# Optimization experiments

Measured on AMD Instinct MI355X. Metric: run time of the kernel, lower is better.

The kernel has to match this reference:

```python
import jax, jax.numpy as jnp
import numpy as np

EPS = 1e-5  # nn.LayerNorm default
H = 16      # n_heads

def _ln(x, s, b):
    m = x.mean(-1, keepdims=True)
    v = x.var(-1, keepdims=True)
    return (x - m) / jnp.sqrt(v + EPS) * s + b


def setup_inputs() -> dict:
    key = jax.random.key(0)
    B, T, D, L, V = 2, 1024, 1024, 6, 32000
    ks = jax.random.split(key, 10)
    def n(k, shape):
        return jax.random.normal(k, shape, dtype=jnp.float32) * 0.02
    return dict(
        x=jax.random.randint(ks[0], (B, T), 0, V),
        tok_emb=n(ks[1], (V, D)),
        pos_emb=n(ks[2], (T, D)),
        Wq=n(ks[3], (L, D, D)), bq=jnp.zeros((L, D), jnp.float32),
        Wk=n(ks[4], (L, D, D)), bk=jnp.zeros((L, D), jnp.float32),
        Wv=n(ks[5], (L, D, D)), bv=jnp.zeros((L, D), jnp.float32),
        ln1_s=jnp.ones((L, D), jnp.float32), ln1_b=jnp.zeros((L, D), jnp.float32),
        W1=n(ks[6], (L, D, 4 * D)), b1=jnp.zeros((L, 4 * D), jnp.float32),
        W2=n(ks[7], (L, 4 * D, D)), b2=jnp.zeros((L, D), jnp.float32),
        ln2_s=jnp.ones((L, D), jnp.float32), ln2_b=jnp.zeros((L, D), jnp.float32),
        Wout=n(ks[8], (D, V)), bout=jnp.zeros((V,), jnp.float32),
    )


def reference(x, tok_emb, pos_emb, Wq, bq, Wk, bk, Wv, bv, ln1_s, ln1_b,
              W1, b1, W2, b2, ln2_s, ln2_b, Wout, bout):
    B, T = x.shape
    D = tok_emb.shape[1]
    hd = D // H
    # embeddings (dropout = identity in eval)
    h = tok_emb[x] + pos_emb[:T]
    # additive causal mask: +1.0 on allowed (tril ones kept), -inf elsewhere,
    # exactly matching torch's tril-ones masked_fill mask
    tril = jnp.tril(jnp.ones((T, T), dtype=h.dtype))
    mask = jnp.where(tril == 0, -jnp.inf, 1.0).astype(h.dtype)
    scale = jnp.asarray(1.0 / np.sqrt(hd), h.dtype)

    def block(h, p):
        wq, bq_, wk, bk_, wv, bv_, l1s, l1b, w1, b1_, w2, b2_, l2s, l2b = p
        def heads(W, b):  # [B,T,D] -> [B,H,T,hd]
            return (h @ W + b).reshape(B, T, H, hd).transpose(0, 2, 1, 3)
        q, k, v = heads(wq, bq_), heads(wk, bk_), heads(wv, bv_)
        s = jnp.einsum('bhqd,bhkd->bhqk', q, k) * scale + mask
        a = jax.nn.softmax(s, axis=-1)
        o = jnp.einsum('bhqk,bhkd->bhqd', a, v).transpose(0, 2, 1, 3).reshape(B, T, D)
        hi = _ln(o + h, l1s, l1b)
        f = jax.nn.relu(hi @ w1 + b1_) @ w2 + b2_
        return _ln(f + hi, l2s, l2b), None

    h, _ = jax.lax.scan(block, h, (Wq, bq, Wk, bk, Wv, bv, ln1_s, ln1_b,
                                   W1, b1, W2, b2, ln2_s, ln2_b))
    return h @ Wout + bout
```

## Files before the change

### kernel.cpp

```cpp
#include <hip/hip_runtime.h>
#include <cstdint>
#include <cstddef>

typedef short bf16x8 __attribute__((ext_vector_type(8)));
typedef float f32x4 __attribute__((ext_vector_type(4)));
typedef unsigned short us4 __attribute__((ext_vector_type(4)));

#define DEV static __device__ __forceinline__

DEV unsigned short f2bf(float f) {
  union { float f; unsigned u; } v; v.f = f;
  unsigned r = v.u + 0x7FFFu + ((v.u >> 16) & 1u);
  return (unsigned short)(r >> 16);
}

DEV void gll16(const void* g, void* l) {
  __builtin_amdgcn_global_load_lds((const __attribute__((address_space(1))) void*)g,
                                   (__attribute__((address_space(3))) void*)l,
                                   16, 0, 0);
}

__global__ __launch_bounds__(256) void embed_kernel(
    const int* __restrict__ x, const float* __restrict__ te,
    const float* __restrict__ pe, float* __restrict__ hf,
    unsigned short* __restrict__ hb) {
  int row = blockIdx.x;
  int t = row & 1023;
  int tok = x[row];
  int tid = threadIdx.x;
  float4 v = ((const float4*)(te + (size_t)tok * 1024))[tid];
  float4 p = ((const float4*)(pe + (size_t)t * 1024))[tid];
  v.x += p.x; v.y += p.y; v.z += p.z; v.w += p.w;
  ((float4*)(hf + (size_t)row * 1024))[tid] = v;
  us4 bv; bv[0] = f2bf(v.x); bv[1] = f2bf(v.y); bv[2] = f2bf(v.z); bv[3] = f2bf(v.w);
  ((us4*)(hb + (size_t)row * 1024))[tid] = bv;
}

__global__ __launch_bounds__(256) void wconv_kernel(
    const float* __restrict__ W, unsigned short* __restrict__ Wt, int K, int N) {
  __shared__ float tile[32][33];
  int n0 = blockIdx.x * 32, k0 = blockIdx.y * 32;
  int tx = threadIdx.x & 31, ty = threadIdx.x >> 5;
#pragma unroll
  for (int i = 0; i < 4; ++i)
    tile[ty * 4 + i][tx] = W[(size_t)(k0 + ty * 4 + i) * N + n0 + tx];
  __syncthreads();
#pragma unroll
  for (int i = 0; i < 4; ++i)
    Wt[(size_t)(n0 + ty * 4 + i) * K + k0 + tx] = f2bf(tile[tx][ty * 4 + i]);
}

__global__ __launch_bounds__(256) void wconv5_kernel(
    const float* __restrict__ Wqf, const float* __restrict__ Wkf,
    const float* __restrict__ Wvf, const float* __restrict__ W1f,
    const float* __restrict__ W2f, unsigned short* __restrict__ wsc) {
  __shared__ float tile[32][33];
  const int bid = blockIdx.x;
  const float* W; unsigned short* Wt; int K, N, b;
  if (bid < 3072) {
    const int s = bid >> 10; b = bid & 1023;
    W = s == 0 ? Wqf : (s == 1 ? Wkf : Wvf);
    Wt = wsc + (size_t)s * 1048576; K = 1024; N = 1024;
  } else if (bid < 7168) {
    b = bid - 3072; W = W1f; Wt = wsc + 3145728; K = 1024; N = 4096;
  } else {
    b = bid - 7168; W = W2f; Wt = wsc + 7340032; K = 4096; N = 1024;
  }
  const int nb = N >> 5;
  const int n0 = (b & (nb - 1)) * 32, k0 = (b / nb) * 32;
  const int tx = threadIdx.x & 31, ty = threadIdx.x >> 5;
#pragma unroll
  for (int i = 0; i < 4; ++i)
    tile[ty * 4 + i][tx] = W[(size_t)(k0 + ty * 4 + i) * N + n0 + tx];
  __syncthreads();
#pragma unroll
  for (int i = 0; i < 4; ++i)
    Wt[(size_t)(n0 + ty * 4 + i) * K + k0 + tx] = f2bf(tile[tx][ty * 4 + i]);
}

template <int EPI>
__global__ __launch_bounds__(512) void gemm5_kernel(
    const unsigned short* __restrict__ A, const unsigned short* __restrict__ Bt,
    const float* __restrict__ bias1, const float* __restrict__ bias2,
    const float* __restrict__ bias3, void* __restrict__ C1,
    void* __restrict__ C2, void* __restrict__ C3,
    int M, int N, int Kstride, int klen, int nbm) {
  constexpr int BM = 256, BN = 128, BK = 64;
  __shared__ unsigned short lA[BM * BK];
  __shared__ unsigned short lB[BN * BK];
  const int tid = threadIdx.x;
  const int wid = tid >> 6, lane = tid & 63;
  const int g = lane >> 4, c = lane & 15;
  const int wm = wid >> 1, wn = wid & 1;

  const int nwg = gridDim.x;
  const int q = nwg >> 3, r = nwg & 7;
  const int xcd = blockIdx.x & 7, jj = blockIdx.x >> 3;
  const int wgid = (xcd < r) ? (xcd * (q + 1) + jj)
                             : (r * (q + 1) + (xcd - r) * q + jj);
  const int bm = (wgid % nbm) * BM;
  const int bn = (wgid / nbm) * BN;
  const int k0 = blockIdx.z * klen;

  f32x4 acc[4][4];
#pragma unroll
  for (int mi = 0; mi < 4; ++mi)
#pragma unroll
    for (int ni = 0; ni < 4; ++ni) acc[mi][ni] = f32x4{0.f, 0.f, 0.f, 0.f};

  for (int kb = 0; kb < klen; kb += BK) {
#pragma unroll
    for (int it = 0; it < 4; ++it) {
      int chunk = it * 512 + tid;
      int row = chunk >> 3, cr = chunk & 7;
      int sc = cr ^ (row & 7);
      gll16(A + (size_t)(bm + row) * Kstride + k0 + kb + sc * 8,
            lA + (size_t)(it * 512 + wid * 64) * 8);
    }
#pragma unroll
    for (int it = 0; it < 2; ++it) {
      int chunk = it * 512 + tid;
      int row = chunk >> 3, cr = chunk & 7;
      int sc = cr ^ (row & 7);
      gll16(Bt + (size_t)(bn + row) * Kstride + k0 + kb + sc * 8,
            lB + (size_t)(it * 512 + wid * 64) * 8);
    }
    __syncthreads();
#pragma unroll
    for (int kk = 0; kk < 2; ++kk) {
      bf16x8 af[4], bfr[4];
#pragma unroll
      for (int mi = 0; mi < 4; ++mi) {
        int row = wm * 64 + mi * 16 + c;
        int ch = (kk * 4 + g) ^ (row & 7);
        af[mi] = *(const bf16x8*)(lA + row * BK + ch * 8);
      }
#pragma unroll
      for (int ni = 0; ni < 4; ++ni) {
        int row = wn * 64 + ni * 16 + c;
        int ch = (kk * 4 + g) ^ (row & 7);
        bfr[ni] = *(const bf16x8*)(lB + row * BK + ch * 8);
      }
#pragma unroll
      for (int mi = 0; mi < 4; ++mi)
#pragma unroll
        for (int ni = 0; ni < 4; ++ni)
          acc[mi][ni] = __builtin_amdgcn_mfma_f32_16x16x32_bf16(
              af[mi], bfr[ni], acc[mi][ni], 0, 0, 0);
    }
    __syncthreads();
  }

  const bool z0 = (blockIdx.z == 0);
#pragma unroll
  for (int mi = 0; mi < 4; ++mi) {
    const int row0 = bm + wm * 64 + mi * 16 + g * 4;
#pragma unroll
    for (int ni = 0; ni < 4; ++ni) {
      const int col = bn + wn * 64 + ni * 16 + c;
      if constexpr (EPI == 0) {
        float* C = (float*)C1 + (size_t)blockIdx.z * M * N;
        const float bv = z0 ? bias1[col] : 0.f;
#pragma unroll
        for (int rr = 0; rr < 4; ++rr)
          C[(size_t)(row0 + rr) * N + col] = acc[mi][ni][rr] + bv;
      } else if constexpr (EPI == 2) {
        const float bv = bias1[col];
#pragma unroll
        for (int rr = 0; rr < 4; ++rr)
          ((unsigned short*)C1)[(size_t)(row0 + rr) * N + col] =
              f2bf(fmaxf(acc[mi][ni][rr] + bv, 0.f));
      } else {
        if (col < 1024) {
          const float bv = bias1[col];
#pragma unroll
          for (int rr = 0; rr < 4; ++rr)
            ((unsigned short*)C1)[(size_t)(row0 + rr) * 1024 + col] =
                f2bf(acc[mi][ni][rr] + bv);
        } else if (col < 2048) {
          const float bv = bias2[col - 1024];
#pragma unroll
          for (int rr = 0; rr < 4; ++rr)
            ((unsigned short*)C2)[(size_t)(row0 + rr) * 1024 + (col - 1024)] =
                f2bf(acc[mi][ni][rr] + bv);
        } else {
          const int cp = col - 2048;
          const float bv = bias3[cp];
          const int hh = cp >> 6, hd = cp & 63;
#pragma unroll
          for (int rr = 0; rr < 4; ++rr) {
            const int row = row0 + rr;
            const int b = row >> 10, t = row & 1023;
            ((unsigned short*)C3)[(size_t)((b * 16 + hh) * 64 + hd) * 1024 + t] =
                f2bf(acc[mi][ni][rr] + bv);
          }
        }
      }
    }
  }
}

__global__ __launch_bounds__(256) void attn_kernel(
    const unsigned short* __restrict__ q, const unsigned short* __restrict__ k,
    const unsigned short* __restrict__ vt, float* __restrict__ o) {
  __shared__ unsigned short lK[128 * 64];
  __shared__ unsigned short lV[64 * 128];
  __shared__ unsigned short lP[4][16 * 128];
  const int tid = threadIdx.x, wid = tid >> 6, lane = tid & 63;
  const int g = lane >> 4, c = lane & 15;
  const int qb = blockIdx.x * 64;
  const int h = blockIdx.y;
  const int b = blockIdx.z;
  const int qw = qb + wid * 16;

  bf16x8 aq[2];
#pragma unroll
  for (int kk = 0; kk < 2; ++kk)
    aq[kk] = *(const bf16x8*)(q + (size_t)(b * 1024 + qw + c) * 1024 + h * 64 + kk * 32 + g * 8);

  float m_run[4], l_run[4];
  f32x4 acc_o[4];
#pragma unroll
  for (int rr = 0; rr < 4; ++rr) { m_run[rr] = -INFINITY; l_run[rr] = 0.f; }
#pragma unroll
  for (int ni = 0; ni < 4; ++ni) acc_o[ni] = f32x4{0.f, 0.f, 0.f, 0.f};

  const int ntiles = (qb >> 7) + 1;
  for (int kt = 0; kt < ntiles; ++kt) {
#pragma unroll
    for (int it = 0; it < 4; ++it) {
      int chunk = it * 256 + tid;
      int row = chunk >> 3, cr = chunk & 7;
      int sc = cr ^ (row & 7);
      gll16(k + (size_t)(b * 1024 + kt * 128 + row) * 1024 + h * 64 + sc * 8,
            lK + (size_t)(it * 256 + wid * 64) * 8);
    }
#pragma unroll
    for (int it = 0; it < 4; ++it) {
      int chunk = it * 256 + tid;
      int row = chunk >> 4, cr = chunk & 15;
      int sc = cr ^ (row & 7);
      gll16(vt + (size_t)((b * 16 + h) * 64 + row) * 1024 + kt * 128 + sc * 8,
            lV + (size_t)(it * 256 + wid * 64) * 8);
    }
    __syncthreads();

    f32x4 accs[8];
#pragma unroll
    for (int ni = 0; ni < 8; ++ni) accs[ni] = f32x4{0.f, 0.f, 0.f, 0.f};
    __builtin_amdgcn_s_setprio(1);
#pragma unroll
    for (int kk = 0; kk < 2; ++kk)
#pragma unroll
      for (int ni = 0; ni < 8; ++ni) {
        int row = ni * 16 + c;
        int ch = (kk * 4 + g) ^ (row & 7);
        bf16x8 kf = *(const bf16x8*)(lK + row * 64 + ch * 8);
        accs[ni] = __builtin_amdgcn_mfma_f32_16x16x32_bf16(aq[kk], kf, accs[ni], 0, 0, 0);
      }
    __builtin_amdgcn_s_setprio(0);

    const bool diag = (kt == ntiles - 1);
    float p[8][4], rowmax[4];
#pragma unroll
    for (int rr = 0; rr < 4; ++rr) rowmax[rr] = -INFINITY;
#pragma unroll
    for (int ni = 0; ni < 8; ++ni)
#pragma unroll
      for (int rr = 0; rr < 4; ++rr) {
        float s = accs[ni][rr] * 0.125f;
        if (diag) {
          int ktok = kt * 128 + ni * 16 + c;
          int qtok = qw + g * 4 + rr;
          if (ktok > qtok) s = -INFINITY;
        }
        p[ni][rr] = s;
        rowmax[rr] = fmaxf(rowmax[rr], s);
      }
#pragma unroll
    for (int mm = 1; mm < 16; mm <<= 1)
#pragma unroll
      for (int rr = 0; rr < 4; ++rr)
        rowmax[rr] = fmaxf(rowmax[rr], __shfl_xor(rowmax[rr], mm, 64));

    float alpha[4];
#pragma unroll
    for (int rr = 0; rr < 4; ++rr) {
      float mn = fmaxf(m_run[rr], rowmax[rr]);
      alpha[rr] = __expf(m_run[rr] - mn);
      m_run[rr] = mn;
    }
#pragma unroll
    for (int ni = 0; ni < 8; ++ni)
#pragma unroll
      for (int rr = 0; rr < 4; ++rr) p[ni][rr] = __expf(p[ni][rr] - m_run[rr]);

    float rowsum[4];
#pragma unroll
    for (int rr = 0; rr < 4; ++rr)
      rowsum[rr] = ((p[0][rr] + p[1][rr]) + (p[2][rr] + p[3][rr])) +
                   ((p[4][rr] + p[5][rr]) + (p[6][rr] + p[7][rr]));
#pragma unroll
    for (int mm = 1; mm < 16; mm <<= 1)
#pragma unroll
      for (int rr = 0; rr < 4; ++rr) rowsum[rr] += __shfl_xor(rowsum[rr], mm, 64);
#pragma unroll
    for (int rr = 0; rr < 4; ++rr) l_run[rr] = l_run[rr] * alpha[rr] + rowsum[rr];
#pragma unroll
    for (int ni = 0; ni < 4; ++ni)
#pragma unroll
      for (int rr = 0; rr < 4; ++rr) acc_o[ni][rr] *= alpha[rr];

#pragma unroll
    for (int ni = 0; ni < 8; ++ni)
#pragma unroll
      for (int rr = 0; rr < 4; ++rr) {
        int qrow = g * 4 + rr;
        int tok = ni * 16 + c;
        int ch = (tok >> 3) ^ (qrow & 7);
        lP[wid][qrow * 128 + ch * 8 + (tok & 7)] = f2bf(p[ni][rr]);
      }

    __builtin_amdgcn_s_setprio(1);
#pragma unroll
    for (int kk = 0; kk < 4; ++kk) {
      int kc = kk * 4 + g;
      int chp = kc ^ (c & 7);
      bf16x8 pa = *(const bf16x8*)(&lP[wid][c * 128 + chp * 8]);
#pragma unroll
      for (int ni = 0; ni < 4; ++ni) {
        int row = ni * 16 + c;
        int ch = kc ^ (row & 7);
        bf16x8 vf = *(const bf16x8*)(lV + row * 128 + ch * 8);
        acc_o[ni] = __builtin_amdgcn_mfma_f32_16x16x32_bf16(pa, vf, acc_o[ni], 0, 0, 0);
      }
    }
    __builtin_amdgcn_s_setprio(0);
    __syncthreads();
  }

#pragma unroll
  for (int ni = 0; ni < 4; ++ni)
#pragma unroll
    for (int rr = 0; rr < 4; ++rr) {
      int row = b * 1024 + qw + g * 4 + rr;
      int col = h * 64 + ni * 16 + c;
      o[(size_t)row * 1024 + col] = acc_o[ni][rr] / l_run[rr];
    }
}

template <int NP>
__global__ __launch_bounds__(256) void ln_add_kernel(
    const float* __restrict__ a1, const float* __restrict__ res,
    const float* __restrict__ s, const float* __restrict__ bb,
    float* __restrict__ out_f, unsigned short* __restrict__ out_b) {
  int row = blockIdx.x, tid = threadIdx.x;
  float4 x = ((const float4*)(a1 + (size_t)row * 1024))[tid];
  float4 rv = ((const float4*)(res + (size_t)row * 1024))[tid];
  x.x += rv.x; x.y += rv.y; x.z += rv.z; x.w += rv.w;
#pragma unroll
  for (int pimg = 1; pimg < NP; ++pimg) {
    float4 x2 = ((const float4*)(a1 + (size_t)pimg * 2097152 + (size_t)row * 1024))[tid];
    x.x += x2.x; x.y += x2.y; x.z += x2.z; x.w += x2.w;
  }
  float sum = x.x + x.y + x.z + x.w;
  float sq = x.x * x.x + x.y * x.y + x.z * x.z + x.w * x.w;
#pragma unroll
  for (int mm = 1; mm < 64; mm <<= 1) {
    sum += __shfl_xor(sum, mm, 64);
    sq += __shfl_xor(sq, mm, 64);
  }
  __shared__ float ssum[4], ssq[4];
  int wid = tid >> 6, lane = tid & 63;
  if (lane == 0) { ssum[wid] = sum; ssq[wid] = sq; }
  __syncthreads();
  sum = ssum[0] + ssum[1] + ssum[2] + ssum[3];
  sq = ssq[0] + ssq[1] + ssq[2] + ssq[3];
  float mean = sum * (1.f / 1024.f);
  float var = sq * (1.f / 1024.f) - mean * mean;
  float rstd = rsqrtf(var + 1e-5f);
  float4 sv = ((const float4*)s)[tid];
  float4 bv = ((const float4*)bb)[tid];
  float4 y;
  y.x = (x.x - mean) * rstd * sv.x + bv.x;
  y.y = (x.y - mean) * rstd * sv.y + bv.y;
  y.z = (x.z - mean) * rstd * sv.z + bv.z;
  y.w = (x.w - mean) * rstd * sv.w + bv.w;
  ((float4*)(out_f + (size_t)row * 1024))[tid] = y;
  us4 ob; ob[0] = f2bf(y.x); ob[1] = f2bf(y.y); ob[2] = f2bf(y.z); ob[3] = f2bf(y.w);
  ((us4*)(out_b + (size_t)row * 1024))[tid] = ob;
}

extern "C" void kernel_launch(void* const* d_in, const int* in_sizes, int n_in,
                              void* d_out, int out_size, void* d_ws, size_t ws_size,
                              hipStream_t stream) {
  const int D = 1024, DFF = 4096, V = 32000, L = 6;
  const int* x = (const int*)d_in[0];
  const float* tok_emb = (const float*)d_in[1];
  const float* pos_emb = (const float*)d_in[2];
  const float* Wq = (const float*)d_in[3];  const float* bq = (const float*)d_in[4];
  const float* Wk = (const float*)d_in[5];  const float* bk = (const float*)d_in[6];
  const float* Wv = (const float*)d_in[7];  const float* bv = (const float*)d_in[8];
  const float* ln1s = (const float*)d_in[9];  const float* ln1b = (const float*)d_in[10];
  const float* W1 = (const float*)d_in[11];  const float* b1 = (const float*)d_in[12];
  const float* W2 = (const float*)d_in[13];  const float* b2 = (const float*)d_in[14];
  const float* ln2s = (const float*)d_in[15]; const float* ln2b = (const float*)d_in[16];
  const float* Wout = (const float*)d_in[17]; const float* bout = (const float*)d_in[18];

  char* ws = (char*)d_ws;
  float* h_res = (float*)(ws + 0);
  float* hi_res = (float*)(ws + 8388608);
  float* tmp = (float*)(ws + 16777216);
  unsigned short* hbf = (unsigned short*)(ws + 25165824);
  unsigned short* qb_ = (unsigned short*)(ws + 29360128);
  unsigned short* kb_ = (unsigned short*)(ws + 33554432);
  unsigned short* vtb = (unsigned short*)(ws + 37748736);
  unsigned short* ffn1 = (unsigned short*)(ws + 41943040);
  unsigned short* wsc = (unsigned short*)(ws + 58720256);
  float* part = (float*)(ws + 58720256 + 25165824);

  embed_kernel<<<2048, 256, 0, stream>>>(x, tok_emb, pos_emb, h_res, hbf);

  for (int l = 0; l < L; ++l) {
    wconv5_kernel<<<11264, 256, 0, stream>>>(
        Wq + (size_t)l * D * D, Wk + (size_t)l * D * D, Wv + (size_t)l * D * D,
        W1 + (size_t)l * D * DFF, W2 + (size_t)l * DFF * D, wsc);
    gemm5_kernel<4><<<192, 512, 0, stream>>>(
        hbf, wsc, bq + l * D, bk + l * D, bv + l * D, qb_, kb_, vtb,
        2048, 3072, D, D, 8);
    attn_kernel<<<dim3(16, 16, 2), 256, 0, stream>>>(qb_, kb_, vtb, tmp);
    ln_add_kernel<1><<<2048, 256, 0, stream>>>(
        tmp, h_res, ln1s + l * D, ln1b + l * D, hi_res, hbf);
    gemm5_kernel<2><<<256, 512, 0, stream>>>(
        hbf, wsc + 3145728, b1 + l * DFF, nullptr, nullptr, ffn1, nullptr, nullptr,
        2048, DFF, D, D, 8);
    gemm5_kernel<0><<<dim3(64, 1, 4), 512, 0, stream>>>(
        ffn1, wsc + 7340032, b2 + l * D, nullptr, nullptr, part, nullptr, nullptr,
        2048, D, DFF, 1024, 8);
    ln_add_kernel<4><<<2048, 256, 0, stream>>>(
        part, hi_res, ln2s + l * D, ln2b + l * D, h_res, hbf);
  }

  wconv_kernel<<<dim3(1000, 32), 256, 0, stream>>>(Wout, wsc, D, V);
  gemm5_kernel<0><<<2000, 512, 0, stream>>>(
      hbf, wsc, bout, nullptr, nullptr, (float*)d_out, nullptr, nullptr,
      2048, V, D, D, 8);
}
```

Baseline: 1.155 ms.

## Fuse weight conversion into embed/LN kernels and use smaller QKV GEMM tile

```diff
diff --git a/kernel.cpp b/kernel.cpp
--- a/kernel.cpp
+++ b/kernel.cpp
@@ -20,14 +20,11 @@
                                    16, 0, 0);
 }
 
-__global__ __launch_bounds__(256) void embed_kernel(
-    const int* __restrict__ x, const float* __restrict__ te,
-    const float* __restrict__ pe, float* __restrict__ hf,
-    unsigned short* __restrict__ hb) {
-  int row = blockIdx.x;
+DEV void embed_body(const int* __restrict__ x, const float* __restrict__ te,
+                    const float* __restrict__ pe, float* __restrict__ hf,
+                    unsigned short* __restrict__ hb, int row, int tid) {
   int t = row & 1023;
   int tok = x[row];
-  int tid = threadIdx.x;
   float4 v = ((const float4*)(te + (size_t)tok * 1024))[tid];
   float4 p = ((const float4*)(pe + (size_t)t * 1024))[tid];
   v.x += p.x; v.y += p.y; v.z += p.z; v.w += p.w;
@@ -36,11 +33,11 @@
   ((us4*)(hb + (size_t)row * 1024))[tid] = bv;
 }
 
-__global__ __launch_bounds__(256) void wconv_kernel(
-    const float* __restrict__ W, unsigned short* __restrict__ Wt, int K, int N) {
-  __shared__ float tile[32][33];
-  int n0 = blockIdx.x * 32, k0 = blockIdx.y * 32;
-  int tx = threadIdx.x & 31, ty = threadIdx.x >> 5;
+DEV void wconv_body(const float* __restrict__ W, unsigned short* __restrict__ Wt,
+                    int K, int N, int b, float (*tile)[33], int tid) {
+  const int nb = N >> 5;
+  const int n0 = (b % nb) * 32, k0 = (b / nb) * 32;
+  const int tx = tid & 31, ty = tid >> 5;
 #pragma unroll
   for (int i = 0; i < 4; ++i)
     tile[ty * 4 + i][tx] = W[(size_t)(k0 + ty * 4 + i) * N + n0 + tx];
@@ -50,311 +47,11 @@
     Wt[(size_t)(n0 + ty * 4 + i) * K + k0 + tx] = f2bf(tile[tx][ty * 4 + i]);
 }
 
-__global__ __launch_bounds__(256) void wconv5_kernel(
-    const float* __restrict__ Wqf, const float* __restrict__ Wkf,
-    const float* __restrict__ Wvf, const float* __restrict__ W1f,
-    const float* __restrict__ W2f, unsigned short* __restrict__ wsc) {
-  __shared__ float tile[32][33];
-  const int bid = blockIdx.x;
-  const float* W; unsigned short* Wt; int K, N, b;
-  if (bid < 3072) {
-    const int s = bid >> 10; b = bid & 1023;
-    W = s == 0 ? Wqf : (s == 1 ? Wkf : Wvf);
-    Wt = wsc + (size_t)s * 1048576; K = 1024; N = 1024;
-  } else if (bid < 7168) {
-    b = bid - 3072; W = W1f; Wt = wsc + 3145728; K = 1024; N = 4096;
-  } else {
-    b = bid - 7168; W = W2f; Wt = wsc + 7340032; K = 4096; N = 1024;
-  }
-  const int nb = N >> 5;
-  const int n0 = (b & (nb - 1)) * 32, k0 = (b / nb) * 32;
-  const int tx = threadIdx.x & 31, ty = threadIdx.x >> 5;
-#pragma unroll
-  for (int i = 0; i < 4; ++i)
-    tile[ty * 4 + i][tx] = W[(size_t)(k0 + ty * 4 + i) * N + n0 + tx];
-  __syncthreads();
-#pragma unroll
-  for (int i = 0; i < 4; ++i)
-    Wt[(size_t)(n0 + ty * 4 + i) * K + k0 + tx] = f2bf(tile[tx][ty * 4 + i]);
-}
-
-template <int EPI>
-__global__ __launch_bounds__(512) void gemm5_kernel(
-    const unsigned short* __restrict__ A, const unsigned short* __restrict__ Bt,
-    const float* __restrict__ bias1, const float* __restrict__ bias2,
-    const float* __restrict__ bias3, void* __restrict__ C1,
-    void* __restrict__ C2, void* __restrict__ C3,
-    int M, int N, int Kstride, int klen, int nbm) {
-  constexpr int BM = 256, BN = 128, BK = 64;
-  __shared__ unsigned short lA[BM * BK];
-  __shared__ unsigned short lB[BN * BK];
-  const int tid = threadIdx.x;
-  const int wid = tid >> 6, lane = tid & 63;
-  const int g = lane >> 4, c = lane & 15;
-  const int wm = wid >> 1, wn = wid & 1;
-
-  const int nwg = gridDim.x;
-  const int q = nwg >> 3, r = nwg & 7;
-  const int xcd = blockIdx.x & 7, jj = blockIdx.x >> 3;
-  const int wgid = (xcd < r) ? (xcd * (q + 1) + jj)
-                             : (r * (q + 1) + (xcd - r) * q + jj);
-  const int bm = (wgid % nbm) * BM;
-  const int bn = (wgid / nbm) * BN;
-  const int k0 = blockIdx.z * klen;
-
-  f32x4 acc[4][4];
-#pragma unroll
-  for (int mi = 0; mi < 4; ++mi)
-#pragma unroll
-    for (int ni = 0; ni < 4; ++ni) acc[mi][ni] = f32x4{0.f, 0.f, 0.f, 0.f};
-
-  for (int kb = 0; kb < klen; kb += BK) {
-#pragma unroll
-    for (int it = 0; it < 4; ++it) {
-      int chunk = it * 512 + tid;
-      int row = chunk >> 3, cr = chunk & 7;
-      int sc = cr ^ (row & 7);
-      gll16(A + (size_t)(bm + row) * Kstride + k0 + kb + sc * 8,
-            lA + (size_t)(it * 512 + wid * 64) * 8);
-    }
-#pragma unroll
-    for (int it = 0; it < 2; ++it) {
-      int chunk = it * 512 + tid;
-      int row = chunk >> 3, cr = chunk & 7;
-      int sc = cr ^ (row & 7);
-      gll16(Bt + (size_t)(bn + row) * Kstride + k0 + kb + sc * 8,
-            lB + (size_t)(it * 512 + wid * 64) * 8);
-    }
-    __syncthreads();
-#pragma unroll
-    for (int kk = 0; kk < 2; ++kk) {
-      bf16x8 af[4], bfr[4];
-#pragma unroll
-      for (int mi = 0; mi < 4; ++mi) {
-        int row = wm * 64 + mi * 16 + c;
-        int ch = (kk * 4 + g) ^ (row & 7);
-        af[mi] = *(const bf16x8*)(lA + row * BK + ch * 8);
-      }
-#pragma unroll
-      for (int ni = 0; ni < 4; ++ni) {
-        int row = wn * 64 + ni * 16 + c;
-        int ch = (kk * 4 + g) ^ (row & 7);
-        bfr[ni] = *(const bf16x8*)(lB + row * BK + ch * 8);
-      }
-#pragma unroll
-      for (int mi = 0; mi < 4; ++mi)
-#pragma unroll
-        for (int ni = 0; ni < 4; ++ni)
-          acc[mi][ni] = __builtin_amdgcn_mfma_f32_16x16x32_bf16(
-              af[mi], bfr[ni], acc[mi][ni], 0, 0, 0);
-    }
-    __syncthreads();
-  }
-
-  const bool z0 = (blockIdx.z == 0);
-#pragma unroll
-  for (int mi = 0; mi < 4; ++mi) {
-    const int row0 = bm + wm * 64 + mi * 16 + g * 4;
-#pragma unroll
-    for (int ni = 0; ni < 4; ++ni) {
-      const int col = bn + wn * 64 + ni * 16 + c;
-      if constexpr (EPI == 0) {
-        float* C = (float*)C1 + (size_t)blockIdx.z * M * N;
-        const float bv = z0 ? bias1[col] : 0.f;
-#pragma unroll
-        for (int rr = 0; rr < 4; ++rr)
-          C[(size_t)(row0 + rr) * N + col] = acc[mi][ni][rr] + bv;
-      } else if constexpr (EPI == 2) {
-        const float bv = bias1[col];
-#pragma unroll
-        for (int rr = 0; rr < 4; ++rr)
-          ((unsigned short*)C1)[(size_t)(row0 + rr) * N + col] =
-              f2bf(fmaxf(acc[mi][ni][rr] + bv, 0.f));
-      } else {
-        if (col < 1024) {
-          const float bv = bias1[col];
-#pragma unroll
-          for (int rr = 0; rr < 4; ++rr)
-            ((unsigned short*)C1)[(size_t)(row0 + rr) * 1024 + col] =
-                f2bf(acc[mi][ni][rr] + bv);
-        } else if (col < 2048) {
-          const float bv = bias2[col - 1024];
-#pragma unroll
-          for (int rr = 0; rr < 4; ++rr)
-            ((unsigned short*)C2)[(size_t)(row0 + rr) * 1024 + (col - 1024)] =
-                f2bf(acc[mi][ni][rr] + bv);
-        } else {
-          const int cp = col - 2048;
-          const float bv = bias3[cp];
-          const int hh = cp >> 6, hd = cp & 63;
-#pragma unroll
-          for (int rr = 0; rr < 4; ++rr) {
-            const int row = row0 + rr;
-            const int b = row >> 10, t = row & 1023;
-            ((unsigned short*)C3)[(size_t)((b * 16 + hh) * 64 + hd) * 1024 + t] =
-                f2bf(acc[mi][ni][rr] + bv);
-          }
-        }
-      }
-    }
-  }
-}
-
-__global__ __launch_bounds__(256) void attn_kernel(
-    const unsigned short* __restrict__ q, const unsigned short* __restrict__ k,
-    const unsigned short* __restrict__ vt, float* __restrict__ o) {
-  __shared__ unsigned short lK[128 * 64];
-  __shared__ unsigned short lV[64 * 128];
-  __shared__ unsigned short lP[4][16 * 128];
-  const int tid = threadIdx.x, wid = tid >> 6, lane = tid & 63;
-  const int g = lane >> 4, c = lane & 15;
-  const int qb = blockIdx.x * 64;
-  const int h = blockIdx.y;
-  const int b = blockIdx.z;
-  const int qw = qb + wid * 16;
-
-  bf16x8 aq[2];
-#pragma unroll
-  for (int kk = 0; kk < 2; ++kk)
-    aq[kk] = *(const bf16x8*)(q + (size_t)(b * 1024 + qw + c) * 1024 + h * 64 + kk * 32 + g * 8);
-
-  float m_run[4], l_run[4];
-  f32x4 acc_o[4];
-#pragma unroll
-  for (int rr = 0; rr < 4; ++rr) { m_run[rr] = -INFINITY; l_run[rr] = 0.f; }
-#pragma unroll
-  for (int ni = 0; ni < 4; ++ni) acc_o[ni] = f32x4{0.f, 0.f, 0.f, 0.f};
-
-  const int ntiles = (qb >> 7) + 1;
-  for (int kt = 0; kt < ntiles; ++kt) {
-#pragma unroll
-    for (int it = 0; it < 4; ++it) {
-      int chunk = it * 256 + tid;
-      int row = chunk >> 3, cr = chunk & 7;
-      int sc = cr ^ (row & 7);
-      gll16(k + (size_t)(b * 1024 + kt * 128 + row) * 1024 + h * 64 + sc * 8,
-            lK + (size_t)(it * 256 + wid * 64) * 8);
-    }
-#pragma unroll
-    for (int it = 0; it < 4; ++it) {
-      int chunk = it * 256 + tid;
-      int row = chunk >> 4, cr = chunk & 15;
-      int sc = cr ^ (row & 7);
-      gll16(vt + (size_t)((b * 16 + h) * 64 + row) * 1024 + kt * 128 + sc * 8,
-            lV + (size_t)(it * 256 + wid * 64) * 8);
-    }
-    __syncthreads();
-
-    f32x4 accs[8];
-#pragma unroll
-    for (int ni = 0; ni < 8; ++ni) accs[ni] = f32x4{0.f, 0.f, 0.f, 0.f};
-    __builtin_amdgcn_s_setprio(1);
-#pragma unroll
-    for (int kk = 0; kk < 2; ++kk)
-#pragma unroll
-      for (int ni = 0; ni < 8; ++ni) {
-        int row = ni * 16 + c;
-        int ch = (kk * 4 + g) ^ (row & 7);
-        bf16x8 kf = *(const bf16x8*)(lK + row * 64 + ch * 8);
-        accs[ni] = __builtin_amdgcn_mfma_f32_16x16x32_bf16(aq[kk], kf, accs[ni], 0, 0, 0);
-      }
-    __builtin_amdgcn_s_setprio(0);
-
-    const bool diag = (kt == ntiles - 1);
-    float p[8][4], rowmax[4];
-#pragma unroll
-    for (int rr = 0; rr < 4; ++rr) rowmax[rr] = -INFINITY;
-#pragma unroll
-    for (int ni = 0; ni < 8; ++ni)
-#pragma unroll
-      for (int rr = 0; rr < 4; ++rr) {
-        float s = accs[ni][rr] * 0.125f;
-        if (diag) {
-          int ktok = kt * 128 + ni * 16 + c;
-          int qtok = qw + g * 4 + rr;
-          if (ktok > qtok) s = -INFINITY;
-        }
-        p[ni][rr] = s;
-        rowmax[rr] = fmaxf(rowmax[rr], s);
-      }
-#pragma unroll
-    for (int mm = 1; mm < 16; mm <<= 1)
-#pragma unroll
-      for (int rr = 0; rr < 4; ++rr)
-        rowmax[rr] = fmaxf(rowmax[rr], __shfl_xor(rowmax[rr], mm, 64));
-
-    float alpha[4];
-#pragma unroll
-    for (int rr = 0; rr < 4; ++rr) {
-      float mn = fmaxf(m_run[rr], rowmax[rr]);
-      alpha[rr] = __expf(m_run[rr] - mn);
-      m_run[rr] = mn;
-    }
-#pragma unroll
-    for (int ni = 0; ni < 8; ++ni)
-#pragma unroll
-      for (int rr = 0; rr < 4; ++rr) p[ni][rr] = __expf(p[ni][rr] - m_run[rr]);
-
-    float rowsum[4];
-#pragma unroll
-    for (int rr = 0; rr < 4; ++rr)
-      rowsum[rr] = ((p[0][rr] + p[1][rr]) + (p[2][rr] + p[3][rr])) +
-                   ((p[4][rr] + p[5][rr]) + (p[6][rr] + p[7][rr]));
-#pragma unroll
-    for (int mm = 1; mm < 16; mm <<= 1)
-#pragma unroll
-      for (int rr = 0; rr < 4; ++rr) rowsum[rr] += __shfl_xor(rowsum[rr], mm, 64);
-#pragma unroll
-    for (int rr = 0; rr < 4; ++rr) l_run[rr] = l_run[rr] * alpha[rr] + rowsum[rr];
-#pragma unroll
-    for (int ni = 0; ni < 4; ++ni)
-#pragma unroll
-      for (int rr = 0; rr < 4; ++rr) acc_o[ni][rr] *= alpha[rr];
-
-#pragma unroll
-    for (int ni = 0; ni < 8; ++ni)
-#pragma unroll
-      for (int rr = 0; rr < 4; ++rr) {
-        int qrow = g * 4 + rr;
-        int tok = ni * 16 + c;
-        int ch = (tok >> 3) ^ (qrow & 7);
-        lP[wid][qrow * 128 + ch * 8 + (tok & 7)] = f2bf(p[ni][rr]);
-      }
-
-    __builtin_amdgcn_s_setprio(1);
-#pragma unroll
-    for (int kk = 0; kk < 4; ++kk) {
-      int kc = kk * 4 + g;
-      int chp = kc ^ (c & 7);
-      bf16x8 pa = *(const bf16x8*)(&lP[wid][c * 128 + chp * 8]);
-#pragma unroll
-      for (int ni = 0; ni < 4; ++ni) {
-        int row = ni * 16 + c;
-        int ch = kc ^ (row & 7);
-        bf16x8 vf = *(const bf16x8*)(lV + row * 128 + ch * 8);
-        acc_o[ni] = __builtin_amdgcn_mfma_f32_16x16x32_bf16(pa, vf, acc_o[ni], 0, 0, 0);
-      }
-    }
-    __builtin_amdgcn_s_setprio(0);
-    __syncthreads();
-  }
-
-#pragma unroll
-  for (int ni = 0; ni < 4; ++ni)
-#pragma unroll
-    for (int rr = 0; rr < 4; ++rr) {
-      int row = b * 1024 + qw + g * 4 + rr;
-      int col = h * 64 + ni * 16 + c;
-      o[(size_t)row * 1024 + col] = acc_o[ni][rr] / l_run[rr];
-    }
-}
-
 template <int NP>
-__global__ __launch_bounds__(256) void ln_add_kernel(
-    const float* __restrict__ a1, const float* __restrict__ res,
-    const float* __restrict__ s, const float* __restrict__ bb,
-    float* __restrict__ out_f, unsigned short* __restrict__ out_b) {
-  int row = blockIdx.x, tid = threadIdx.x;
+DEV void ln_body(const float* __restrict__ a1, const float* __restrict__ res,
+                 const float* __restrict__ s, const float* __restrict__ bb,
+                 float* __restrict__ out_f, unsigned short* __restrict__ out_b,
+                 int row, int tid, float* red) {
   float4 x = ((const float4*)(a1 + (size_t)row * 1024))[tid];
   float4 rv = ((const float4*)(res + (size_t)row * 1024))[tid];
   x.x += rv.x; x.y += rv.y; x.z += rv.z; x.w += rv.w;
@@ -370,12 +67,11 @@
     sum += __shfl_xor(sum, mm, 64);
     sq += __shfl_xor(sq, mm, 64);
   }
-  __shared__ float ssum[4], ssq[4];
   int wid = tid >> 6, lane = tid & 63;
-  if (lane == 0) { ssum[wid] = sum; ssq[wid] = sq; }
+  if (lane == 0) { red[wid] = sum; red[4 + wid] = sq; }
   __syncthreads();
-  sum = ssum[0] + ssum[1] + ssum[2] + ssum[3];
-  sq = ssq[0] + ssq[1] + ssq[2] + ssq[3];
+  sum = red[0] + red[1] + red[2] + red[3];
+  sq = red[4] + red[5] + red[6] + red[7];
   float mean = sum * (1.f / 1024.f);
   float var = sq * (1.f / 1024.f) - mean * mean;
   float rstd = rsqrtf(var + 1e-5f);
@@ -389,6 +85,345 @@
   ((float4*)(out_f + (size_t)row * 1024))[tid] = y;
   us4 ob; ob[0] = f2bf(y.x); ob[1] = f2bf(y.y); ob[2] = f2bf(y.z); ob[3] = f2bf(y.w);
   ((us4*)(out_b + (size_t)row * 1024))[tid] = ob;
+}
+
+DEV void wconv5_select(int bid, const float* Wqf, const float* Wkf,
+                       const float* Wvf, const float* W1f, const float* W2f,
+                       unsigned short* wsc, float (*tile)[33], int tid) {
+  const float* W; unsigned short* Wt; int K, N, b;
+  if (bid < 3072) {
+    const int sgl = bid >> 10; b = bid & 1023;
+    W = sgl == 0 ? Wqf : (sgl == 1 ? Wkf : Wvf);
+    Wt = wsc + (size_t)sgl * 1048576; K = 1024; N = 1024;
+  } else if (bid < 7168) {
+    b = bid - 3072; W = W1f; Wt = wsc + 3145728; K = 1024; N = 4096;
+  } else {
+    b = bid - 7168; W = W2f; Wt = wsc + 7340032; K = 4096; N = 1024;
+  }
+  wconv_body(W, Wt, K, N, b, tile, tid);
+}
+
+__global__ __launch_bounds__(256) void embed_wconv_kernel(
+    const int* __restrict__ x, const float* __restrict__ te,
+    const float* __restrict__ pe, float* __restrict__ hf,
+    unsigned short* __restrict__ hb,
+    const float* __restrict__ Wqf, const float* __restrict__ Wkf,
+    const float* __restrict__ Wvf, const float* __restrict__ W1f,
+    const float* __restrict__ W2f, unsigned short* __restrict__ wsc) {
+  __shared__ float tile[32][33];
+  const int bid = blockIdx.x;
+  if (bid < 2048) {
+    embed_body(x, te, pe, hf, hb, bid, threadIdx.x);
+    return;
+  }
+  wconv5_select(bid - 2048, Wqf, Wkf, Wvf, W1f, W2f, wsc, tile, threadIdx.x);
+}
+
+template <int NP>
+__global__ __launch_bounds__(256) void ln_wconv5_kernel(
+    const float* __restrict__ a1, const float* __restrict__ res,
+    const float* __restrict__ s, const float* __restrict__ bb,
+    float* __restrict__ out_f, unsigned short* __restrict__ out_b,
+    const float* __restrict__ Wqf, const float* __restrict__ Wkf,
+    const float* __restrict__ Wvf, const float* __restrict__ W1f,
+    const float* __restrict__ W2f, unsigned short* __restrict__ wsc) {
+  __shared__ float tile[32][33];
+  __shared__ float red[8];
+  const int bid = blockIdx.x;
+  if (bid < 2048) {
+    ln_body<NP>(a1, res, s, bb, out_f, out_b, bid, threadIdx.x, red);
+    return;
+  }
+  wconv5_select(bid - 2048, Wqf, Wkf, Wvf, W1f, W2f, wsc, tile, threadIdx.x);
+}
+
+template <int NP>
+__global__ __launch_bounds__(256) void ln_add_kernel(
+    const float* __restrict__ a1, const float* __restrict__ res,
+    const float* __restrict__ s, const float* __restrict__ bb,
+    float* __restrict__ out_f, unsigned short* __restrict__ out_b) {
+  __shared__ float red[8];
+  ln_body<NP>(a1, res, s, bb, out_f, out_b, blockIdx.x, threadIdx.x, red);
+}
+
+__global__ __launch_bounds__(256) void wconv_kernel(
+    const float* __restrict__ W, unsigned short* __restrict__ Wt, int K, int N) {
+  __shared__ float tile[32][33];
+  const int nb = N >> 5;
+  wconv_body(W, Wt, K, N, blockIdx.y * nb + blockIdx.x, tile, threadIdx.x);
+}
+
+template <int BM, int EPI>
+__global__ __launch_bounds__(512) void gemm5_kernel(
+    const unsigned short* __restrict__ A, const unsigned short* __restrict__ Bt,
+    const float* __restrict__ bias1, const float* __restrict__ bias2,
+    const float* __restrict__ bias3, void* __restrict__ C1,
+    void* __restrict__ C2, void* __restrict__ C3,
+    int M, int N, int Kstride, int klen, int nbm) {
+  constexpr int BN = 128, BK = 64;
+  constexpr int MFR = BM / 64;
+  constexpr int AIT = BM / 64;
+  __shared__ unsigned short lA[BM * BK];
+  __shared__ unsigned short lB[BN * BK];
+  const int tid = threadIdx.x;
+  const int wid = tid >> 6, lane = tid & 63;
+  const int g = lane >> 4, c = lane & 15;
+  const int wm = wid >> 1, wn = wid & 1;
+
+  const int nwg = gridDim.x;
+  const int q = nwg >> 3, r = nwg & 7;
+  const int xcd = blockIdx.x & 7, jj = blockIdx.x >> 3;
+  const int wgid = (xcd < r) ? (xcd * (q + 1) + jj)
+                             : (r * (q + 1) + (xcd - r) * q + jj);
+  const int bm = (wgid % nbm) * BM;
+  const int bn = (wgid / nbm) * BN;
+  const int k0 = blockIdx.z * klen;
+
+  f32x4 acc[MFR][4];
+#pragma unroll
+  for (int mi = 0; mi < MFR; ++mi)
+#pragma unroll
+    for (int ni = 0; ni < 4; ++ni) acc[mi][ni] = f32x4{0.f, 0.f, 0.f, 0.f};
+
+  for (int kb = 0; kb < klen; kb += BK) {
+#pragma unroll
+    for (int it = 0; it < AIT; ++it) {
+      int chunk = it * 512 + tid;
+      int row = chunk >> 3, cr = chunk & 7;
+      int sc = cr ^ (row & 7);
+      gll16(A + (size_t)(bm + row) * Kstride + k0 + kb + sc * 8,
+            lA + (size_t)(it * 512 + wid * 64) * 8);
+    }
+#pragma unroll
+    for (int it = 0; it < 2; ++it) {
+      int chunk = it * 512 + tid;
+      int row = chunk >> 3, cr = chunk & 7;
+      int sc = cr ^ (row & 7);
+      gll16(Bt + (size_t)(bn + row) * Kstride + k0 + kb + sc * 8,
+            lB + (size_t)(it * 512 + wid * 64) * 8);
+    }
+    __syncthreads();
+#pragma unroll
+    for (int kk = 0; kk < 2; ++kk) {
+      bf16x8 af[MFR], bfr[4];
+#pragma unroll
+      for (int mi = 0; mi < MFR; ++mi) {
+        int row = wm * (BM / 4) + mi * 16 + c;
+        int ch = (kk * 4 + g) ^ (row & 7);
+        af[mi] = *(const bf16x8*)(lA + row * BK + ch * 8);
+      }
+#pragma unroll
+      for (int ni = 0; ni < 4; ++ni) {
+        int row = wn * 64 + ni * 16 + c;
+        int ch = (kk * 4 + g) ^ (row & 7);
+        bfr[ni] = *(const bf16x8*)(lB + row * BK + ch * 8);
+      }
+#pragma unroll
+      for (int mi = 0; mi < MFR; ++mi)
+#pragma unroll
+        for (int ni = 0; ni < 4; ++ni)
+          acc[mi][ni] = __builtin_amdgcn_mfma_f32_16x16x32_bf16(
+              af[mi], bfr[ni], acc[mi][ni], 0, 0, 0);
+    }
+    __syncthreads();
+  }
+
+  const bool z0 = (blockIdx.z == 0);
+#pragma unroll
+  for (int mi = 0; mi < MFR; ++mi) {
+    const int row0 = bm + wm * (BM / 4) + mi * 16 + g * 4;
+#pragma unroll
+    for (int ni = 0; ni < 4; ++ni) {
+      const int col = bn + wn * 64 + ni * 16 + c;
+      if constexpr (EPI == 0) {
+        float* C = (float*)C1 + (size_t)blockIdx.z * M * N;
+        const float bv = z0 ? bias1[col] : 0.f;
+#pragma unroll
+        for (int rr = 0; rr < 4; ++rr)
+          C[(size_t)(row0 + rr) * N + col] = acc[mi][ni][rr] + bv;
+      } else if constexpr (EPI == 2) {
+        const float bv = bias1[col];
+#pragma unroll
+        for (int rr = 0; rr < 4; ++rr)
+          ((unsigned short*)C1)[(size_t)(row0 + rr) * N + col] =
+              f2bf(fmaxf(acc[mi][ni][rr] + bv, 0.f));
+      } else {
+        if (col < 1024) {
+          const float bv = bias1[col];
+#pragma unroll
+          for (int rr = 0; rr < 4; ++rr)
+            ((unsigned short*)C1)[(size_t)(row0 + rr) * 1024 + col] =
+                f2bf(acc[mi][ni][rr] + bv);
+        } else if (col < 2048) {
+          const float bv = bias2[col - 1024];
+#pragma unroll
+          for (int rr = 0; rr < 4; ++rr)
+            ((unsigned short*)C2)[(size_t)(row0 + rr) * 1024 + (col - 1024)] =
+                f2bf(acc[mi][ni][rr] + bv);
+        } else {
+          const int cp = col - 2048;
+          const float bv = bias3[cp];
+          const int hh = cp >> 6, hd = cp & 63;
+#pragma unroll
+          for (int rr = 0; rr < 4; ++rr) {
+            const int row = row0 + rr;
+            const int b = row >> 10, t = row & 1023;
+            ((unsigned short*)C3)[(size_t)((b * 16 + hh) * 64 + hd) * 1024 + t] =
+                f2bf(acc[mi][ni][rr] + bv);
+          }
+        }
+      }
+    }
+  }
+}
+
+__global__ __launch_bounds__(256) void attn_kernel(
+    const unsigned short* __restrict__ q, const unsigned short* __restrict__ k,
+    const unsigned short* __restrict__ vt, float* __restrict__ o) {
+  __shared__ unsigned short lK[128 * 64];
+  __shared__ unsigned short lV[64 * 128];
+  __shared__ unsigned short lP[4][16 * 128];
+  const int tid = threadIdx.x, wid = tid >> 6, lane = tid & 63;
+  const int g = lane >> 4, c = lane & 15;
+  const int qb = blockIdx.x * 64;
+  const int h = blockIdx.y;
+  const int b = blockIdx.z;
+  const int qw = qb + wid * 16;
+
+  bf16x8 aq[2];
+#pragma unroll
+  for (int kk = 0; kk < 2; ++kk)
+    aq[kk] = *(const bf16x8*)(q + (size_t)(b * 1024 + qw + c) * 1024 + h * 64 + kk * 32 + g * 8);
+
+  float m_run[4], l_run[4];
+  f32x4 acc_o[4];
+#pragma unroll
+  for (int rr = 0; rr < 4; ++rr) { m_run[rr] = -INFINITY; l_run[rr] = 0.f; }
+#pragma unroll
+  for (int ni = 0; ni < 4; ++ni) acc_o[ni] = f32x4{0.f, 0.f, 0.f, 0.f};
+
+  const int ntiles = (qb >> 7) + 1;
+  for (int kt = 0; kt < ntiles; ++kt) {
+#pragma unroll
+    for (int it = 0; it < 4; ++it) {
+      int chunk = it * 256 + tid;
+      int row = chunk >> 3, cr = chunk & 7;
+      int sc = cr ^ (row & 7);
+      gll16(k + (size_t)(b * 1024 + kt * 128 + row) * 1024 + h * 64 + sc * 8,
+            lK + (size_t)(it * 256 + wid * 64) * 8);
+    }
+#pragma unroll
+    for (int it = 0; it < 4; ++it) {
+      int chunk = it * 256 + tid;
+      int row = chunk >> 4, cr = chunk & 15;
+      int sc = cr ^ (row & 7);
+      gll16(vt + (size_t)((b * 16 + h) * 64 + row) * 1024 + kt * 128 + sc * 8,
+            lV + (size_t)(it * 256 + wid * 64) * 8);
+    }
+    __syncthreads();
+
+    f32x4 accs[8];
+#pragma unroll
+    for (int ni = 0; ni < 8; ++ni) accs[ni] = f32x4{0.f, 0.f, 0.f, 0.f};
+    __builtin_amdgcn_s_setprio(1);
+#pragma unroll
+    for (int kk = 0; kk < 2; ++kk)
+#pragma unroll
+      for (int ni = 0; ni < 8; ++ni) {
+        int row = ni * 16 + c;
+        int ch = (kk * 4 + g) ^ (row & 7);
+        bf16x8 kf = *(const bf16x8*)(lK + row * 64 + ch * 8);
+        accs[ni] = __builtin_amdgcn_mfma_f32_16x16x32_bf16(aq[kk], kf, accs[ni], 0, 0, 0);
+      }
+    __builtin_amdgcn_s_setprio(0);
+
+    const bool diag = (kt == ntiles - 1);
+    float p[8][4], rowmax[4];
+#pragma unroll
+    for (int rr = 0; rr < 4; ++rr) rowmax[rr] = -INFINITY;
+#pragma unroll
+    for (int ni = 0; ni < 8; ++ni)
+#pragma unroll
+      for (int rr = 0; rr < 4; ++rr) {
+        float s = accs[ni][rr] * 0.125f;
+        if (diag) {
+          int ktok = kt * 128 + ni * 16 + c;
+          int qtok = qw + g * 4 + rr;
+          if (ktok > qtok) s = -INFINITY;
+        }
+        p[ni][rr] = s;
+        rowmax[rr] = fmaxf(rowmax[rr], s);
+      }
+#pragma unroll
+    for (int mm = 1; mm < 16; mm <<= 1)
+#pragma unroll
+      for (int rr = 0; rr < 4; ++rr)
+        rowmax[rr] = fmaxf(rowmax[rr], __shfl_xor(rowmax[rr], mm, 64));
+
+    float alpha[4];
+#pragma unroll
+    for (int rr = 0; rr < 4; ++rr) {
+      float mn = fmaxf(m_run[rr], rowmax[rr]);
+      alpha[rr] = __expf(m_run[rr] - mn);
+      m_run[rr] = mn;
+    }
+#pragma unroll
+    for (int ni = 0; ni < 8; ++ni)
+#pragma unroll
+      for (int rr = 0; rr < 4; ++rr) p[ni][rr] = __expf(p[ni][rr] - m_run[rr]);
+
+    float rowsum[4];
+#pragma unroll
+    for (int rr = 0; rr < 4; ++rr)
+      rowsum[rr] = ((p[0][rr] + p[1][rr]) + (p[2][rr] + p[3][rr])) +
+                   ((p[4][rr] + p[5][rr]) + (p[6][rr] + p[7][rr]));
+#pragma unroll
+    for (int mm = 1; mm < 16; mm <<= 1)
+#pragma unroll
+      for (int rr = 0; rr < 4; ++rr) rowsum[rr] += __shfl_xor(rowsum[rr], mm, 64);
+#pragma unroll
+    for (int rr = 0; rr < 4; ++rr) l_run[rr] = l_run[rr] * alpha[rr] + rowsum[rr];
+#pragma unroll
+    for (int ni = 0; ni < 4; ++ni)
+#pragma unroll
+      for (int rr = 0; rr < 4; ++rr) acc_o[ni][rr] *= alpha[rr];
+
+#pragma unroll
+    for (int ni = 0; ni < 8; ++ni)
+#pragma unroll
+      for (int rr = 0; rr < 4; ++rr) {
+        int qrow = g * 4 + rr;
+        int tok = ni * 16 + c;
+        int ch = (tok >> 3) ^ (qrow & 7);
+        lP[wid][qrow * 128 + ch * 8 + (tok & 7)] = f2bf(p[ni][rr]);
+      }
+
+    __builtin_amdgcn_s_setprio(1);
+#pragma unroll
+    for (int kk = 0; kk < 4; ++kk) {
+      int kc = kk * 4 + g;
+      int chp = kc ^ (c & 7);
+      bf16x8 pa = *(const bf16x8*)(&lP[wid][c * 128 + chp * 8]);
+#pragma unroll
+      for (int ni = 0; ni < 4; ++ni) {
+        int row = ni * 16 + c;
+        int ch = kc ^ (row & 7);
+        bf16x8 vf = *(const bf16x8*)(lV + row * 128 + ch * 8);
+        acc_o[ni] = __builtin_amdgcn_mfma_f32_16x16x32_bf16(pa, vf, acc_o[ni], 0, 0, 0);
+      }
+    }
+    __builtin_amdgcn_s_setprio(0);
+    __syncthreads();
+  }
+
+#pragma unroll
+  for (int ni = 0; ni < 4; ++ni)
+#pragma unroll
+    for (int rr = 0; rr < 4; ++rr) {
+      int row = b * 1024 + qw + g * 4 + rr;
+      int col = h * 64 + ni * 16 + c;
+      o[(size_t)row * 1024 + col] = acc_o[ni][rr] / l_run[rr];
+    }
 }
 
 extern "C" void kernel_launch(void* const* d_in, const int* in_sizes, int n_in,
@@ -419,30 +454,37 @@
   unsigned short* wsc = (unsigned short*)(ws + 58720256);
   float* part = (float*)(ws + 58720256 + 25165824);
 
-  embed_kernel<<<2048, 256, 0, stream>>>(x, tok_emb, pos_emb, h_res, hbf);
+  embed_wconv_kernel<<<13312, 256, 0, stream>>>(
+      x, tok_emb, pos_emb, h_res, hbf,
+      Wq, Wk, Wv, W1, W2, wsc);
 
   for (int l = 0; l < L; ++l) {
-    wconv5_kernel<<<11264, 256, 0, stream>>>(
-        Wq + (size_t)l * D * D, Wk + (size_t)l * D * D, Wv + (size_t)l * D * D,
-        W1 + (size_t)l * D * DFF, W2 + (size_t)l * DFF * D, wsc);
-    gemm5_kernel<4><<<192, 512, 0, stream>>>(
+    gemm5_kernel<128, 4><<<384, 512, 0, stream>>>(
         hbf, wsc, bq + l * D, bk + l * D, bv + l * D, qb_, kb_, vtb,
-        2048, 3072, D, D, 8);
+        2048, 3072, D, D, 16);
     attn_kernel<<<dim3(16, 16, 2), 256, 0, stream>>>(qb_, kb_, vtb, tmp);
     ln_add_kernel<1><<<2048, 256, 0, stream>>>(
         tmp, h_res, ln1s + l * D, ln1b + l * D, hi_res, hbf);
-    gemm5_kernel<2><<<256, 512, 0, stream>>>(
+    gemm5_kernel<256, 2><<<256, 512, 0, stream>>>(
         hbf, wsc + 3145728, b1 + l * DFF, nullptr, nullptr, ffn1, nullptr, nullptr,
         2048, DFF, D, D, 8);
-    gemm5_kernel<0><<<dim3(64, 1, 4), 512, 0, stream>>>(
+    gemm5_kernel<256, 0><<<dim3(64, 1, 4), 512, 0, stream>>>(
         ffn1, wsc + 7340032, b2 + l * D, nullptr, nullptr, part, nullptr, nullptr,
         2048, D, DFF, 1024, 8);
-    ln_add_kernel<4><<<2048, 256, 0, stream>>>(
-        part, hi_res, ln2s + l * D, ln2b + l * D, h_res, hbf);
+    if (l < L - 1) {
+      ln_wconv5_kernel<4><<<13312, 256, 0, stream>>>(
+          part, hi_res, ln2s + l * D, ln2b + l * D, h_res, hbf,
+          Wq + (size_t)(l + 1) * D * D, Wk + (size_t)(l + 1) * D * D,
+          Wv + (size_t)(l + 1) * D * D, W1 + (size_t)(l + 1) * D * DFF,
+          W2 + (size_t)(l + 1) * DFF * D, wsc);
+    } else {
+      ln_add_kernel<4><<<2048, 256, 0, stream>>>(
+          part, hi_res, ln2s + l * D, ln2b + l * D, h_res, hbf);
+    }
   }
 
   wconv_kernel<<<dim3(1000, 32), 256, 0, stream>>>(Wout, wsc, D, V);
-  gemm5_kernel<0><<<2000, 512, 0, stream>>>(
+  gemm5_kernel<256, 0><<<2000, 512, 0, stream>>>(
       hbf, wsc, bout, nullptr, nullptr, (float*)d_out, nullptr, nullptr,
       2048, V, D, D, 8);
 }
```

After: 1.084 ms, median of 3. 6.1% less time.
